# Kernel tuning notes

Measured on AMD Instinct MI355X. Metric: run time of the kernel, lower is better.

Reference implementation:

```python
import jax, jax.numpy as jnp
import numpy as np

TIME_LAG, PRE_LEN, STATIONS, SAMPLES = 12, 3, 40, 38
B, H, DM, DFF = 4, 8, 512, 2048
L = STATIONS * SAMPLES          # 1520 tokens fed to Informer
SAMPLE_K = 40                   # factor(5)*ceil(ln L); also n_top selected queries
N_ENC = 2


def sinusoid(length, d):
    pos = np.arange(length, dtype=np.float32)[:, None]
    i = np.arange(d)[None, :]
    ang = pos / np.power(10000.0, (2 * (i // 2)) / d)
    pe = np.where(i % 2 == 0, np.sin(ang), np.cos(ang)).astype(np.float32)
    return jnp.asarray(pe)


def layernorm(x, g, b, eps=1e-5):
    mu = x.mean(-1, keepdims=True)
    var = ((x - mu) ** 2).mean(-1, keepdims=True)
    return (x - mu) * jax.lax.rsqrt(var + eps) * g + b


def heads(x):
    b, l, d = x.shape
    return x.reshape(b, l, H, d // H).transpose(0, 2, 1, 3)


def unheads(x):
    b, h, l, dh = x.shape
    return x.transpose(0, 2, 1, 3).reshape(b, l, h * dh)


def prob_attention(Q, K, V, idx):
    # ProbSparse attention (Informer). Q,K,V: [B,H,L,Dh]; idx: [L, SAMPLE_K] sampled key ids.
    b, h, l, dh = Q.shape
    def col(ic):  # one sampled key per query; avoids [B,H,L,S,Dh] gather blowup
        return jnp.einsum('bhld,bhld->bhl', Q, K[:, :, ic, :])
    qk_s = jnp.moveaxis(jax.lax.map(col, idx.T), 0, -1)       # [B,H,L,SAMPLE_K]
    M = qk_s.max(-1) - qk_s.sum(-1) / l                        # sparsity measure
    _, top = jax.lax.top_k(M, SAMPLE_K)                        # [B,H,n_top]
    Qr = jnp.take_along_axis(Q, top[..., None], axis=2)        # [B,H,n_top,Dh]
    scores = jnp.einsum('bhud,bhkd->bhuk', Qr, K) / jnp.sqrt(jnp.float32(dh))
    ctx_top = jax.nn.softmax(scores, axis=-1) @ V              # [B,H,n_top,Dh]
    ctx = jnp.broadcast_to(V.mean(axis=2, keepdims=True), Q.shape)
    bi = jnp.arange(b)[:, None, None]
    hi = jnp.arange(h)[None, :, None]
    return ctx.at[bi, hi, top].set(ctx_top)


def full_attention(Q, K, V):
    scores = jnp.einsum('bhqd,bhkd->bhqk', Q, K) / jnp.sqrt(jnp.float32(Q.shape[-1]))
    return jax.nn.softmax(scores, axis=-1) @ V


def ffn(x, Wa, ba, Wb, bb):
    return jax.nn.gelu(x @ Wa + ba) @ Wb + bb


def _forward(inflow, P, samp_idx):
    x = inflow[:, 2:2 + TIME_LAG].reshape(B, -1, TIME_LAG)     # [B,L,T] (row-major, same as torch)
    pe = sinusoid(L, DM)
    enc = x @ P['W_emb_e'] + P['b_emb_e'] + pe
    for i in range(N_ENC):
        qkv = enc @ P['enc_Wqkv'][i] + P['enc_bqkv'][i]
        q, k, v = jnp.split(qkv, 3, axis=-1)
        ctx = unheads(prob_attention(heads(q), heads(k), heads(v), samp_idx[i]))
        enc = layernorm(enc + ctx @ P['enc_Wo'][i] + P['enc_bo'][i], P['enc_ln1_g'][i], P['enc_ln1_b'][i])
        y = ffn(enc, P['enc_Wf1'][i], P['enc_bf1'][i], P['enc_Wf2'][i], P['enc_bf2'][i])
        enc = layernorm(enc + y, P['enc_ln2_g'][i], P['enc_ln2_b'][i])
    enc = layernorm(enc, P['enc_norm_g'], P['enc_norm_b'])
    dec = x @ P['W_emb_d'] + P['b_emb_d'] + pe
    qkv = dec @ P['dec_Wqkv'] + P['dec_bqkv']
    q, k, v = jnp.split(qkv, 3, axis=-1)
    ctx = unheads(prob_attention(heads(q), heads(k), heads(v), samp_idx[2]))
    dec = layernorm(dec + ctx @ P['dec_Wo_s'] + P['dec_bo_s'], P['dec_ln1_g'], P['dec_ln1_b'])
    qc = dec @ P['dec_Wq_c'] + P['dec_bq_c']
    kc, vc = jnp.split(enc @ P['dec_Wkv_c'] + P['dec_bkv_c'], 2, axis=-1)
    ctx = unheads(full_attention(heads(qc), heads(kc), heads(vc)))
    dec = layernorm(dec + ctx @ P['dec_Wo_c'] + P['dec_bo_c'], P['dec_ln2_g'], P['dec_ln2_b'])
    y = ffn(dec, P['dec_Wf1'], P['dec_bf1'], P['dec_Wf2'], P['dec_bf2'])
    dec = layernorm(dec + y, P['dec_ln3_g'], P['dec_ln3_b'])
    out = dec @ P['W_proj'] + P['b_proj'] + x                  # Informer output + residual
    out = jax.nn.relu(out @ P['W1'] + P['b1']) @ P['W3'] + P['b3']
    return out.reshape(B, PRE_LEN, STATIONS, SAMPLES)


def setup_inputs():
    key = jax.random.key(0)
    keys = iter(jax.random.split(key, 80))
    def w(*shape):
        return jax.random.normal(next(keys), shape, jnp.float32) * 0.02
    def zeros(*shape):
        return jnp.zeros(shape, jnp.float32)
    def ones(*shape):
        return jnp.ones(shape, jnp.float32)
    inp = dict(
        flow=zeros(1), ODRate=zeros(1), adj=zeros(1), external=zeros(1),
        inflow=jax.random.normal(next(keys), (B, 2 + TIME_LAG, STATIONS, SAMPLES), jnp.float32),
        W_emb_e=w(TIME_LAG, DM), b_emb_e=zeros(DM),
        W_emb_d=w(TIME_LAG, DM), b_emb_d=zeros(DM),
        enc_Wqkv=w(N_ENC, DM, 3 * DM), enc_bqkv=zeros(N_ENC, 3 * DM),
        enc_Wo=w(N_ENC, DM, DM), enc_bo=zeros(N_ENC, DM),
        enc_ln1_g=ones(N_ENC, DM), enc_ln1_b=zeros(N_ENC, DM),
        enc_Wf1=w(N_ENC, DM, DFF), enc_bf1=zeros(N_ENC, DFF),
        enc_Wf2=w(N_ENC, DFF, DM), enc_bf2=zeros(N_ENC, DM),
        enc_ln2_g=ones(N_ENC, DM), enc_ln2_b=zeros(N_ENC, DM),
        enc_norm_g=ones(DM), enc_norm_b=zeros(DM),
        dec_Wqkv=w(DM, 3 * DM), dec_bqkv=zeros(3 * DM),
        dec_Wo_s=w(DM, DM), dec_bo_s=zeros(DM),
        dec_ln1_g=ones(DM), dec_ln1_b=zeros(DM),
        dec_Wq_c=w(DM, DM), dec_bq_c=zeros(DM),
        dec_Wkv_c=w(DM, 2 * DM), dec_bkv_c=zeros(2 * DM),
        dec_Wo_c=w(DM, DM), dec_bo_c=zeros(DM),
        dec_ln2_g=ones(DM), dec_ln2_b=zeros(DM),
        dec_Wf1=w(DM, DFF), dec_bf1=zeros(DFF),
        dec_Wf2=w(DFF, DM), dec_bf2=zeros(DM),
        dec_ln3_g=ones(DM), dec_ln3_b=zeros(DM),
        W_proj=w(DM, TIME_LAG), b_proj=zeros(TIME_LAG),
        W1=w(TIME_LAG, 128), b1=zeros(128),
        W3=w(128, PRE_LEN), b3=zeros(PRE_LEN),
        samp_idx=jax.random.randint(next(keys), (3, L, SAMPLE_K), 0, L, jnp.int32),
    )
    return inp


def reference(flow, inflow, ODRate, adj, external, W_emb_e, b_emb_e, W_emb_d, b_emb_d, enc_Wqkv, enc_bqkv, enc_Wo, enc_bo, enc_ln1_g, enc_ln1_b, enc_Wf1, enc_bf1, enc_Wf2, enc_bf2, enc_ln2_g, enc_ln2_b, enc_norm_g, enc_norm_b, dec_Wqkv, dec_bqkv, dec_Wo_s, dec_bo_s, dec_ln1_g, dec_ln1_b, dec_Wq_c, dec_bq_c, dec_Wkv_c, dec_bkv_c, dec_Wo_c, dec_bo_c, dec_ln2_g, dec_ln2_b, dec_Wf1, dec_bf1, dec_Wf2, dec_bf2, dec_ln3_g, dec_ln3_b, W_proj, b_proj, W1, b1, W3, b3, samp_idx):
    args = locals()
    skip = ('flow', 'inflow', 'ODRate', 'adj', 'external', 'samp_idx')
    P = {k: v for k, v in args.items() if k not in skip}
    return _forward(inflow, P, samp_idx)
```

## Files before the change

kernel.cpp:

```cpp
#include <hip/hip_runtime.h>
#include <math.h>

#define B_ 4
#define H_ 8
#define L_ 1520
#define DM_ 512
#define DFF_ 2048
#define SK_ 40
#define ML_ (B_*L_)
#define MP_ 6144
#define LP_ 1536

typedef unsigned short u16;
typedef short s8v __attribute__((ext_vector_type(8)));
typedef float f4 __attribute__((ext_vector_type(4)));

__device__ __forceinline__ u16 f2b(float x) {
  union { float f; unsigned u; } c; c.f = x;
  unsigned r = c.u + 0x7FFFu + ((c.u >> 16) & 1u);
  return (u16)(r >> 16);
}
__device__ __forceinline__ float b2f(u16 h) {
  union { unsigned u; float f; } c; c.u = ((unsigned)h) << 16;
  return c.f;
}
__device__ __forceinline__ unsigned cvt_pk(float a, float b) {
  unsigned r;
  asm volatile("v_cvt_pk_bf16_f32 %0, %1, %2" : "=v"(r) : "v"(a), "v"(b));
  return r;
}
__device__ __forceinline__ float gelu_tanh(float x) {
  float x3 = x * x * x;
  return 0.5f * x * (1.f + tanhf(0.79788456080286536f * (x + 0.044715f * x3)));
}
__device__ __forceinline__ int xswz(int bid, int cpx) {
  return (bid & 7) * cpx + (bid >> 3);
}

__global__ __launch_bounds__(256) void pe_kernel(float* __restrict__ pe) {
  int idx = blockIdx.x * 256 + threadIdx.x;
  if (idx >= L_ * DM_) return;
  int pos = idx / DM_, i = idx % DM_;
  double expo = (double)(2 * (i / 2)) / (double)DM_;
  double ang = (double)pos / pow(10000.0, expo);
  pe[idx] = (i & 1) ? (float)cos(ang) : (float)sin(ang);
}

__global__ __launch_bounds__(256) void extract_x(const float* __restrict__ inflow,
                                                 float* __restrict__ X) {
  int idx = blockIdx.x * 256 + threadIdx.x;
  if (idx >= ML_ * 12) return;
  int b = idx / (L_ * 12);
  int rem = idx - b * (L_ * 12);
  X[idx] = inflow[(size_t)b * 14 * L_ + 2 * L_ + rem];
}

struct CvtArgs {
  const float* src[15];
  unsigned cumt[16];
  unsigned lk[15];
};
__global__ __launch_bounds__(256) void cvt_all(CvtArgs a, u16* __restrict__ dst) {
  __shared__ float tl[32][33];
  int bt = blockIdx.x;
  int s = 0;
#pragma unroll
  for (int i = 1; i < 15; ++i) s += (bt >= (int)a.cumt[i]);
  int lt = bt - a.cumt[s];
  unsigned lk = a.lk[s];
  unsigned K = 1u << lk;
  unsigned N = ((a.cumt[s + 1] - a.cumt[s]) << 10) >> lk;
  unsigned tiles_n = N >> 5;
  unsigned k0 = (lt / tiles_n) * 32, n0 = (lt % tiles_n) * 32;
  const float* src = a.src[s];
  int r = threadIdx.x >> 5, c = threadIdx.x & 31;
#pragma unroll
  for (int i = 0; i < 4; ++i)
    tl[r + 8 * i][c] = src[(size_t)(k0 + r + 8 * i) * N + n0 + c];
  __syncthreads();
  u16* d = dst + ((size_t)a.cumt[s] << 10);
#pragma unroll
  for (int i = 0; i < 4; ++i)
    d[(size_t)(n0 + r + 8 * i) * K + k0 + c] = f2b(tl[c][r + 8 * i]);
}

__global__ __launch_bounds__(256) void embed_fused(
    const float* __restrict__ X, const float* __restrict__ W,
    const float* __restrict__ bias, const float* __restrict__ PE,
    float* __restrict__ ACT, u16* __restrict__ ACTb) {
  int row = blockIdx.x * 4 + (threadIdx.x >> 6);
  int lane = threadIdx.x & 63;
  int d0 = lane * 8;
  if (row >= ML_) {
    s8v z = {0, 0, 0, 0, 0, 0, 0, 0};
    *(s8v*)(ACTb + (size_t)row * DM_ + d0) = z;
    return;
  }
  int prow = row % L_;
  f4 a0 = *(const f4*)(bias + d0);
  f4 a1 = *(const f4*)(bias + d0 + 4);
  a0 += *(const f4*)(PE + (size_t)prow * DM_ + d0);
  a1 += *(const f4*)(PE + (size_t)prow * DM_ + d0 + 4);
  const float* xr = X + (size_t)row * 12;
#pragma unroll
  for (int t = 0; t < 12; ++t) {
    float xv = xr[t];
    a0 += xv * *(const f4*)(W + (size_t)t * DM_ + d0);
    a1 += xv * *(const f4*)(W + (size_t)t * DM_ + d0 + 4);
  }
  float* dst = ACT + (size_t)row * DM_ + d0;
  *(f4*)dst = a0;
  *(f4*)(dst + 4) = a1;
  unsigned ob[4];
  ob[0] = cvt_pk(a0[0], a0[1]); ob[1] = cvt_pk(a0[2], a0[3]);
  ob[2] = cvt_pk(a1[0], a1[1]); ob[3] = cvt_pk(a1[2], a1[3]);
  *(s8v*)(ACTb + (size_t)row * DM_ + d0) = *(s8v*)ob;
}

__global__ __launch_bounds__(256) void head_fused(
    const float* __restrict__ DEC, const float* __restrict__ X,
    const float* __restrict__ Wp, const float* __restrict__ bp,
    const float* __restrict__ W1, const float* __restrict__ b1,
    const float* __restrict__ W3, const float* __restrict__ b3,
    float* __restrict__ out) {
  int row = blockIdx.x * 4 + (threadIdx.x >> 6);
  int lane = threadIdx.x & 63;
  int d0 = lane * 8;
  const float* dec = DEC + (size_t)row * DM_ + d0;
  f4 v0 = *(const f4*)dec;
  f4 v1 = *(const f4*)(dec + 4);
  float pj[12];
#pragma unroll
  for (int j = 0; j < 12; ++j) pj[j] = 0.f;
#pragma unroll
  for (int i = 0; i < 8; ++i) {
    float dv = (i < 4) ? v0[i] : v1[i - 4];
    const float* wr = Wp + (size_t)(d0 + i) * 12;
#pragma unroll
    for (int j = 0; j < 12; ++j) pj[j] += dv * wr[j];
  }
  for (int off = 32; off; off >>= 1) {
#pragma unroll
    for (int j = 0; j < 12; ++j) pj[j] += __shfl_xor(pj[j], off);
  }
  float o12[12];
#pragma unroll
  for (int j = 0; j < 12; ++j) o12[j] = pj[j] + bp[j] + X[(size_t)row * 12 + j];
  int k0 = lane * 2;
  float h0 = b1[k0], h1 = b1[k0 + 1];
#pragma unroll
  for (int j = 0; j < 12; ++j) {
    h0 += o12[j] * W1[j * 128 + k0];
    h1 += o12[j] * W1[j * 128 + k0 + 1];
  }
  h0 = fmaxf(h0, 0.f);
  h1 = fmaxf(h1, 0.f);
  float op[3];
#pragma unroll
  for (int p = 0; p < 3; ++p)
    op[p] = h0 * W3[k0 * 3 + p] + h1 * W3[(k0 + 1) * 3 + p];
  for (int off = 32; off; off >>= 1) {
#pragma unroll
    for (int p = 0; p < 3; ++p) op[p] += __shfl_xor(op[p], off);
  }
  if (lane == 0) {
#pragma unroll
    for (int p = 0; p < 3; ++p) out[(size_t)row * 3 + p] = op[p] + b3[p];
  }
}

template<int BM>
__global__ __launch_bounds__(256) void gemm_bf16(
    const u16* __restrict__ A, const u16* __restrict__ Bt,
    const float* __restrict__ bias, const float* __restrict__ res,
    float* __restrict__ Cf, u16* __restrict__ Cb,
    int N, int K, int act) {
  __shared__ __align__(16) u16 As[BM * 32];
  __shared__ __align__(16) u16 Bs[128 * 32];
  constexpr int MI = BM / 32;
  const int nwg = gridDim.x * gridDim.y;
  const int lin = blockIdx.y * gridDim.x + blockIdx.x;
  const int o = xswz(lin, nwg >> 3);
  const int bxi = o % gridDim.x, byi = o / gridDim.x;
  const int t = threadIdx.x, w = t >> 6, lane = t & 63;
  const int lg = lane >> 4, li = lane & 15;
  const int bm = byi * BM, bn = bxi * 128;
  const int wr = (w >> 1) * (BM / 2), wc = (w & 1) * 64;
  f4 acc[MI][4];
#pragma unroll
  for (int i = 0; i < MI; ++i)
#pragma unroll
    for (int j = 0; j < 4; ++j) acc[i][j] = f4{0.f, 0.f, 0.f, 0.f};
  const int rB = w * 32 + (lane >> 2);
  const int rA = (BM == 128) ? rB : (w * 16 + (lane >> 2));
  const int ps = lane & 3;
  for (int k0 = 0; k0 < K; k0 += 32) {
    if (BM == 128) {
#pragma unroll
      for (int j = 0; j < 2; ++j) {
        int r = rA + j * 16;
        int ls = ps ^ ((r >> 1) & 3);
        __builtin_amdgcn_global_load_lds(
            (const __attribute__((address_space(1))) void*)(A + (size_t)(bm + r) * K + k0 + ls * 8),
            (__attribute__((address_space(3))) void*)(As + (w * 32 + j * 16) * 32),
            16, 0, 0);
      }
    } else {
      int ls = ps ^ ((rA >> 1) & 3);
      __builtin_amdgcn_global_load_lds(
          (const __attribute__((address_space(1))) void*)(A + (size_t)(bm + rA) * K + k0 + ls * 8),
          (__attribute__((address_space(3))) void*)(As + (w * 16) * 32),
          16, 0, 0);
    }
#pragma unroll
    for (int j = 0; j < 2; ++j) {
      int r = rB + j * 16;
      int ls = ps ^ ((r >> 1) & 3);
      __builtin_amdgcn_global_load_lds(
          (const __attribute__((address_space(1))) void*)(Bt + (size_t)(bn + r) * K + k0 + ls * 8),
          (__attribute__((address_space(3))) void*)(Bs + (w * 32 + j * 16) * 32),
          16, 0, 0);
    }
    __syncthreads();
    s8v af[MI], bf[4];
#pragma unroll
    for (int f = 0; f < MI; ++f) {
      int ra = wr + f * 16 + li;
      af[f] = *(const s8v*)(As + ra * 32 + ((lg ^ ((ra >> 1) & 3)) * 8));
    }
#pragma unroll
    for (int f = 0; f < 4; ++f) {
      int rb = wc + f * 16 + li;
      bf[f] = *(const s8v*)(Bs + rb * 32 + ((lg ^ ((rb >> 1) & 3)) * 8));
    }
#pragma unroll
    for (int fi = 0; fi < MI; ++fi)
#pragma unroll
      for (int fj = 0; fj < 4; ++fj)
        acc[fi][fj] = __builtin_amdgcn_mfma_f32_16x16x32_bf16(af[fi], bf[fj], acc[fi][fj], 0, 0, 0);
    __syncthreads();
  }
#pragma unroll
  for (int fi = 0; fi < MI; ++fi)
#pragma unroll
    for (int fj = 0; fj < 4; ++fj)
#pragma unroll
      for (int r = 0; r < 4; ++r) {
        int row = bm + wr + fi * 16 + lg * 4 + r;
        int col = bn + wc + fj * 16 + li;
        float v = acc[fi][fj][r] + bias[col];
        if (res && row < ML_) v += res[(size_t)row * N + col];
        if (act == 1) v = gelu_tanh(v);
        if (Cf && row < ML_) Cf[(size_t)row * N + col] = v;
        if (Cb) Cb[(size_t)row * N + col] = f2b(v);
      }
}

__global__ __launch_bounds__(256) void layernorm_ip(float* __restrict__ Xb,
                                                    const float* __restrict__ g,
                                                    const float* __restrict__ bta,
                                                    u16* __restrict__ outb) {
  int row = blockIdx.x * 4 + (threadIdx.x >> 6);
  int lane = threadIdx.x & 63;
  float* x = Xb + (size_t)row * DM_;
  f4 a = *(f4*)(x + lane * 8);
  f4 b = *(f4*)(x + lane * 8 + 4);
  float s = a[0] + a[1] + a[2] + a[3] + b[0] + b[1] + b[2] + b[3];
  for (int off = 32; off; off >>= 1) s += __shfl_xor(s, off);
  float mu = s * (1.f / 512.f);
  float vs = 0.f;
#pragma unroll
  for (int i = 0; i < 4; ++i) { a[i] -= mu; b[i] -= mu; vs += a[i] * a[i] + b[i] * b[i]; }
  for (int off = 32; off; off >>= 1) vs += __shfl_xor(vs, off);
  float rs = rsqrtf(vs * (1.f / 512.f) + 1e-5f);
  f4 g0 = *(const f4*)(g + lane * 8), g1 = *(const f4*)(g + lane * 8 + 4);
  f4 c0 = *(const f4*)(bta + lane * 8), c1 = *(const f4*)(bta + lane * 8 + 4);
  float r0 = a[0] * rs * g0[0] + c0[0];
  float r1 = a[1] * rs * g0[1] + c0[1];
  float r2 = a[2] * rs * g0[2] + c0[2];
  float r3 = a[3] * rs * g0[3] + c0[3];
  float r4 = b[0] * rs * g1[0] + c1[0];
  float r5 = b[1] * rs * g1[1] + c1[1];
  float r6 = b[2] * rs * g1[2] + c1[2];
  float r7 = b[3] * rs * g1[3] + c1[3];
  x[lane * 8 + 0] = r0; x[lane * 8 + 1] = r1; x[lane * 8 + 2] = r2; x[lane * 8 + 3] = r3;
  x[lane * 8 + 4] = r4; x[lane * 8 + 5] = r5; x[lane * 8 + 6] = r6; x[lane * 8 + 7] = r7;
  unsigned ob[4];
  ob[0] = cvt_pk(r0, r1); ob[1] = cvt_pk(r2, r3);
  ob[2] = cvt_pk(r4, r5); ob[3] = cvt_pk(r6, r7);
  *(s8v*)(outb + (size_t)row * DM_ + lane * 8) = *(s8v*)ob;
}

__global__ __launch_bounds__(256) void probM(const u16* __restrict__ qkv,
                                             const int* __restrict__ sidx,
                                             float* __restrict__ Mout) {
  int wid = threadIdx.x / 64, lane = threadIdx.x % 64;
  int o = xswz(blockIdx.x, (B_ * H_ * L_ / 4) >> 3);
  int g = o * 4 + wid;
  int l = g % L_;
  int bh = g / L_;
  int h = bh % H_, b = bh / H_;
  __shared__ float qs[4][64];
  qs[wid][lane] = b2f(qkv[((size_t)b * L_ + l) * 1536 + h * 64 + lane]);
  __syncthreads();
  float dot = 0.f;
  if (lane < SK_) {
    int ks = sidx[l * SK_ + lane];
    const u16* kr = qkv + ((size_t)b * L_ + ks) * 1536 + 512 + h * 64;
#pragma unroll
    for (int j = 0; j < 8; ++j) {
      s8v v = *(const s8v*)(kr + j * 8);
#pragma unroll
      for (int i = 0; i < 8; ++i) dot += qs[wid][j * 8 + i] * b2f((u16)v[i]);
    }
  }
  float vmax = (lane < SK_) ? dot : -INFINITY;
  float vsum = (lane < SK_) ? dot : 0.f;
  for (int off = 32; off; off >>= 1) {
    vmax = fmaxf(vmax, __shfl_xor(vmax, off));
    vsum += __shfl_xor(vsum, off);
  }
  if (lane == 0) Mout[g] = vmax - vsum / (float)L_;
}

__global__ __launch_bounds__(256) void radix_topk(const float* __restrict__ Mv,
                                                  int* __restrict__ top) {
  const int bh = blockIdx.x;
  const int t = threadIdx.x;
  const int base = t * 6;
  unsigned key[6];
#pragma unroll
  for (int i = 0; i < 6; ++i) {
    int ix = base + i;
    unsigned k = 0u;
    if (ix < L_) {
      union { float f; unsigned u; } c; c.f = Mv[(size_t)bh * L_ + ix];
      k = c.u ^ ((c.u & 0x80000000u) ? 0xFFFFFFFFu : 0x80000000u);
    }
    key[i] = k;
  }
  __shared__ int wred[4];
  __shared__ int s_a[256], s_b[256];
  unsigned prefix = 0u;
  for (int b = 31; b >= 0; --b) {
    unsigned cand = prefix | (1u << b);
    int c = 0;
#pragma unroll
    for (int i = 0; i < 6; ++i) c += (key[i] >= cand);
    for (int off = 32; off; off >>= 1) c += __shfl_xor(c, off);
    if ((t & 63) == 0) wred[t >> 6] = c;
    __syncthreads();
    int tot = wred[0] + wred[1] + wred[2] + wred[3];
    if (tot >= SK_) prefix = cand;
    __syncthreads();
  }
  const unsigned T = prefix;
  int gt = 0, tie = 0;
#pragma unroll
  for (int i = 0; i < 6; ++i) { gt += (key[i] > T); tie += (key[i] == T); }
  s_a[t] = gt; s_b[t] = tie;
  __syncthreads();
  for (int off = 1; off < 256; off <<= 1) {
    int va = (t >= off) ? s_a[t - off] : 0;
    int vb = (t >= off) ? s_b[t - off] : 0;
    __syncthreads();
    s_a[t] += va; s_b[t] += vb;
    __syncthreads();
  }
  const int n_strict = s_a[255];
  const int gt_base = s_a[t] - gt;
  const int tie_base = s_b[t] - tie;
  const int need = SK_ - n_strict;
  int lgt = 0, ltie = 0;
#pragma unroll
  for (int i = 0; i < 6; ++i) {
    int ix = base + i;
    if (key[i] > T) {
      top[bh * SK_ + gt_base + lgt] = ix; ++lgt;
    } else if (key[i] == T) {
      int r = tie_base + ltie; ++ltie;
      if (r < need) top[bh * SK_ + n_strict + r] = ix;
    }
  }
}

__global__ __launch_bounds__(256) void transpose_v(const u16* __restrict__ src,
                                                   int stride, int voff0,
                                                   u16* __restrict__ VT) {
  int o = xswz(blockIdx.x, (B_ * H_ * 24) >> 3);
  int kt = o % 24, bh = o / 24;
  int h = bh & 7, b = bh >> 3;
  int kb = kt * 64;
  __shared__ u16 tile[64][72];
  int t = threadIdx.x;
#pragma unroll
  for (int rr = 0; rr < 2; ++rr) {
    int slot = rr * 256 + t;
    int key = slot >> 3, d = (slot & 7) * 8;
    int gk = kb + key; if (gk >= L_) gk = L_ - 1;
    s8v v = *(const s8v*)(src + (size_t)(b * L_ + gk) * stride + voff0 + h * 64 + d);
    *(s8v*)(&tile[key][d]) = v;
  }
  __syncthreads();
  int dim = t >> 2, k0 = (t & 3) * 16;
  u16 buf[16];
#pragma unroll
  for (int i = 0; i < 16; ++i) {
    int key = k0 + i;
    buf[i] = (kb + key < L_) ? tile[key][dim] : (u16)0;
  }
  *(s8v*)(VT + ((size_t)bh * 64 + dim) * LP_ + kb + k0) = *(s8v*)buf;
  *(s8v*)(VT + ((size_t)bh * 64 + dim) * LP_ + kb + k0 + 8) = *(s8v*)(buf + 8);
}

template<int MODE>
__global__ __launch_bounds__(256) void flash_attn(
    const u16* __restrict__ Qm, const u16* __restrict__ Kg,
    const u16* __restrict__ VT, const int* __restrict__ top,
    float* __restrict__ POf, u16* POa, u16* POb,
    float* __restrict__ PM, float* __restrict__ PL) {
  constexpr int QSTR = (MODE == 0) ? 512 : 1536;
  constexpr int KSTR = (MODE == 0) ? 512 : 1536;
  constexpr int TILES = (MODE == 0) ? 12 : 3;
  constexpr int NB = (MODE == 0) ? 48 : 8;
  __shared__ __align__(16) u16 Kt[64 * 64];
  __shared__ __align__(16) u16 Vt[64 * 64];
  __shared__ __align__(16) unsigned Xch[4][576];
  const int o = xswz(blockIdx.x, (B_ * H_ * NB) >> 3);
  int bh, sp, qb;
  if (MODE == 0) {
    bh = o / 48; int rem = o % 48; qb = rem >> 1; sp = rem & 1;
  } else {
    bh = o / 8; sp = o % 8; qb = 0;
  }
  const int h = bh & 7, b = bh >> 3;
  const int qoff = h * 64;
  const int koff = ((MODE == 0) ? 0 : 512) + h * 64;
  const int t = threadIdx.x, w = t >> 6, lane = t & 63;
  const int lg = lane >> 4, li = lane & 15;
  const u16* vtg = VT + (size_t)bh * 64 * LP_;
  unsigned* xw = Xch[w];
  u16* xw16 = (u16*)xw;

  int qrow;
  if (MODE == 0) {
    int q = qb * 64 + w * 16 + li;
    qrow = b * L_ + ((q < L_) ? q : (L_ - 1));
  } else {
    int u = w * 16 + li; if (u >= SK_) u = SK_ - 1;
    qrow = b * L_ + top[bh * SK_ + u];
  }
  s8v qf0 = *(const s8v*)(Qm + (size_t)qrow * QSTR + qoff + lg * 8);
  s8v qf1 = *(const s8v*)(Qm + (size_t)qrow * QSTR + qoff + 32 + lg * 8);

  f4 o4[4];
#pragma unroll
  for (int n = 0; n < 4; ++n) o4[n] = f4{0.f, 0.f, 0.f, 0.f};
  float m_run = -INFINITY, l_run = 0.f;
  const int kt0 = sp * TILES;
  const int skey = lane >> 3;
  const int sslot = lane & 7;

#pragma unroll 1
  for (int ki = 0; ki < TILES; ++ki) {
    const int kb = (kt0 + ki) * 64;
#pragma unroll
    for (int j = 0; j < 2; ++j) {
      int row = w * 16 + j * 8 + skey;
      int gk = kb + row; if (gk >= L_) gk = L_ - 1;
      int ck = sslot ^ (row & 7);
      __builtin_amdgcn_global_load_lds(
          (const __attribute__((address_space(1))) void*)(Kg + (size_t)(b * L_ + gk) * KSTR + koff + ck * 8),
          (__attribute__((address_space(3))) void*)(Kt + (w * 16 + j * 8) * 64),
          16, 0, 0);
      int cv = sslot ^ (row & 7);
      __builtin_amdgcn_global_load_lds(
          (const __attribute__((address_space(1))) void*)(vtg + (size_t)row * LP_ + kb + cv * 8),
          (__attribute__((address_space(3))) void*)(Vt + (w * 16 + j * 8) * 64),
          16, 0, 0);
    }
    __syncthreads();
    f4 s[4];
#pragma unroll
    for (int c = 0; c < 4; ++c) {
      int key = c * 16 + li;
      s8v kf = *(const s8v*)(Kt + key * 64 + ((lg ^ (key & 7)) * 8));
      s8v kg2 = *(const s8v*)(Kt + key * 64 + (((lg + 4) ^ (key & 7)) * 8));
      f4 z = f4{0.f, 0.f, 0.f, 0.f};
      z = __builtin_amdgcn_mfma_f32_16x16x32_bf16(kf, qf0, z, 0, 0, 0);
      z = __builtin_amdgcn_mfma_f32_16x16x32_bf16(kg2, qf1, z, 0, 0, 0);
      s[c] = z * 0.125f;
    }
    if (kb + 64 > L_) {
#pragma unroll
      for (int c = 0; c < 4; ++c)
#pragma unroll
        for (int r = 0; r < 4; ++r)
          if (kb + c * 16 + lg * 4 + r >= L_) s[c][r] = -INFINITY;
    }
    float tm = -INFINITY;
#pragma unroll
    for (int c = 0; c < 4; ++c)
      tm = fmaxf(tm, fmaxf(fmaxf(s[c][0], s[c][1]), fmaxf(s[c][2], s[c][3])));
    tm = fmaxf(tm, __shfl_xor(tm, 16));
    tm = fmaxf(tm, __shfl_xor(tm, 32));
    float mn = fmaxf(m_run, tm);
    float sc = __expf(m_run - mn);
    float p[4][4];
    float rs = 0.f;
#pragma unroll
    for (int c = 0; c < 4; ++c)
#pragma unroll
      for (int r = 0; r < 4; ++r) { p[c][r] = __expf(s[c][r] - mn); rs += p[c][r]; }
    rs += __shfl_xor(rs, 16);
    rs += __shfl_xor(rs, 32);
    l_run = l_run * sc + rs;
    m_run = mn;
#pragma unroll
    for (int n = 0; n < 4; ++n) o4[n] *= sc;
#pragma unroll
    for (int c = 0; c < 4; ++c)
#pragma unroll
      for (int rp = 0; rp < 2; ++rp)
        xw[li * 36 + c * 8 + lg * 2 + rp] = cvt_pk(p[c][2 * rp], p[c][2 * rp + 1]);
    s8v pb0 = *(const s8v*)(xw + li * 36 + lg * 4);
    s8v pb1 = *(const s8v*)(xw + li * 36 + 16 + lg * 4);
#pragma unroll
    for (int n = 0; n < 4; ++n) {
      int dim = n * 16 + li;
      s8v vb0 = *(const s8v*)(Vt + dim * 64 + ((lg ^ (dim & 7)) * 8));
      o4[n] = __builtin_amdgcn_mfma_f32_16x16x32_bf16(vb0, pb0, o4[n], 0, 0, 0);
    }
#pragma unroll
    for (int n = 0; n < 4; ++n) {
      int dim = n * 16 + li;
      s8v vb1 = *(const s8v*)(Vt + dim * 64 + (((lg + 4) ^ (dim & 7)) * 8));
      o4[n] = __builtin_amdgcn_mfma_f32_16x16x32_bf16(vb1, pb1, o4[n], 0, 0, 0);
    }
    __syncthreads();
  }

  if (MODE == 0) {
#pragma unroll
    for (int n = 0; n < 4; ++n)
#pragma unroll
      for (int rp = 0; rp < 2; ++rp)
        xw[li * 36 + n * 8 + lg * 2 + rp] = cvt_pk(o4[n][2 * rp], o4[n][2 * rp + 1]);
    u16* PO = sp ? POb : POa;
    const int pid = (bh * 24 + qb) * 2 + sp;
    int q_local = lane >> 2, d0 = (lane & 3) * 16;
    int q = qb * 64 + w * 16 + q_local;
    s8v v0 = *(const s8v*)(xw16 + q_local * 72 + d0);
    s8v v1 = *(const s8v*)(xw16 + q_local * 72 + d0 + 8);
    if (q < L_) {
      u16* dst = PO + ((size_t)(b * L_ + q)) * DM_ + qoff + d0;
      *(s8v*)dst = v0;
      *(s8v*)(dst + 8) = v1;
    }
    if (lg == 0) {
      PM[pid * 64 + w * 16 + li] = m_run;
      PL[pid * 64 + w * 16 + li] = l_run;
    }
  } else {
    int base = (bh * 8 + sp) * 64 + w * 16 + li;
#pragma unroll
    for (int n = 0; n < 4; ++n)
#pragma unroll
      for (int r = 0; r < 4; ++r)
        POf[(size_t)base * 64 + n * 16 + lg * 4 + r] = o4[n][r];
    if (lg == 0) {
      PM[base] = m_run;
      PL[base] = l_run;
    }
  }
}

__global__ __launch_bounds__(256) void combine_cross(const u16* __restrict__ PO0,
                                                     const float* __restrict__ PM,
                                                     const float* __restrict__ PL,
                                                     u16* ctxb) {
  int idx = blockIdx.x * 256 + threadIdx.x;
  int row = idx >> 9, col = idx & 511;
  int b = row / L_, q = row - b * L_;
  int h = col >> 6;
  int bh = b * 8 + h, qbk = q >> 6, qi = q & 63;
  int p0 = ((bh * 24 + qbk) * 2) * 64 + qi;
  float m0 = PM[p0], m1 = PM[p0 + 64];
  float l0 = PL[p0], l1 = PL[p0 + 64];
  float M = fmaxf(m0, m1);
  float w0 = __expf(m0 - M), w1 = __expf(m1 - M);
  float inv = 1.f / (w0 * l0 + w1 * l1);
  float o0 = b2f(PO0[idx]);
  float o1 = b2f(ctxb[idx]);
  ctxb[idx] = f2b((w0 * o0 + w1 * o1) * inv);
}

__global__ __launch_bounds__(256) void combine_prob_scatter(
    const float* __restrict__ PO, const float* __restrict__ PM,
    const float* __restrict__ PL, const int* __restrict__ top,
    u16* __restrict__ ctxb) {
  int bh = blockIdx.x;
  int t = threadIdx.x;
  int u = t >> 2, dg = (t & 3) * 16;
  if (u >= SK_) return;
  float M = -INFINITY;
  for (int s = 0; s < 8; ++s) M = fmaxf(M, PM[(bh * 8 + s) * 64 + u]);
  float wgt[8];
  float den = 0.f;
  for (int s = 0; s < 8; ++s) {
    wgt[s] = __expf(PM[(bh * 8 + s) * 64 + u] - M);
    den += wgt[s] * PL[(bh * 8 + s) * 64 + u];
  }
  float inv = 1.f / den;
  int h = bh & 7, b = bh >> 3;
  int l = top[bh * SK_ + u];
  u16* dst = ctxb + ((size_t)(b * L_ + l)) * DM_ + h * 64;
  for (int d = dg; d < dg + 16; ++d) {
    float acc = 0.f;
    for (int s = 0; s < 8; ++s) acc += wgt[s] * PO[(((size_t)bh * 8 + s) * 64 + u) * 64 + d];
    dst[d] = f2b(acc * inv);
  }
}

__global__ __launch_bounds__(256) void vmean_part(const u16* __restrict__ qkv,
                                                  float* __restrict__ part) {
  int g = xswz(blockIdx.x, (B_ * H_ * 8) >> 3);
  int bh = g >> 3, seg = g & 7;
  int h = bh & 7, b = bh >> 3;
  int lane = threadIdx.x & 63, grp = threadIdx.x >> 6;
  int k0 = seg * 190, k1 = k0 + 190;
  float acc = 0.f;
  for (int k = k0 + grp; k < k1; k += 4)
    acc += b2f(qkv[((size_t)b * L_ + k) * 1536 + 1024 + h * 64 + lane]);
  __shared__ float pv[4][64];
  pv[grp][lane] = acc;
  __syncthreads();
  if (threadIdx.x < 64)
    part[g * 64 + threadIdx.x] =
        pv[0][threadIdx.x] + pv[1][threadIdx.x] + pv[2][threadIdx.x] + pv[3][threadIdx.x];
}

__global__ __launch_bounds__(256) void fill_ctx(const float* __restrict__ part,
                                                u16* __restrict__ ctxb) {
  int idx = blockIdx.x * 256 + threadIdx.x;
  int d = idx % 64;
  int h = (idx / 64) % H_;
  int b = idx / (L_ * DM_);
  int bh = b * 8 + h;
  float s = 0.f;
#pragma unroll
  for (int seg = 0; seg < 8; ++seg) s += part[(bh * 8 + seg) * 64 + d];
  ctxb[idx] = f2b(s * (1.f / (float)L_));
}

extern "C" void kernel_launch(void* const* d_in, const int* in_sizes, int n_in,
                              void* d_out, int out_size, void* d_ws, size_t ws_size,
                              hipStream_t stream) {
  const float* inflow   = (const float*)d_in[4];
  const float* W_emb_e  = (const float*)d_in[5];
  const float* b_emb_e  = (const float*)d_in[6];
  const float* W_emb_d  = (const float*)d_in[7];
  const float* b_emb_d  = (const float*)d_in[8];
  const float* enc_Wqkv = (const float*)d_in[9];
  const float* enc_bqkv = (const float*)d_in[10];
  const float* enc_Wo   = (const float*)d_in[11];
  const float* enc_bo   = (const float*)d_in[12];
  const float* enc_ln1g = (const float*)d_in[13];
  const float* enc_ln1b = (const float*)d_in[14];
  const float* enc_Wf1  = (const float*)d_in[15];
  const float* enc_bf1  = (const float*)d_in[16];
  const float* enc_Wf2  = (const float*)d_in[17];
  const float* enc_bf2  = (const float*)d_in[18];
  const float* enc_ln2g = (const float*)d_in[19];
  const float* enc_ln2b = (const float*)d_in[20];
  const float* enc_ng   = (const float*)d_in[21];
  const float* enc_nb   = (const float*)d_in[22];
  const float* dec_Wqkv = (const float*)d_in[23];
  const float* dec_bqkv = (const float*)d_in[24];
  const float* dec_Wo_s = (const float*)d_in[25];
  const float* dec_bo_s = (const float*)d_in[26];
  const float* dec_ln1g = (const float*)d_in[27];
  const float* dec_ln1b = (const float*)d_in[28];
  const float* dec_Wq_c = (const float*)d_in[29];
  const float* dec_bq_c = (const float*)d_in[30];
  const float* dec_Wkv  = (const float*)d_in[31];
  const float* dec_bkv  = (const float*)d_in[32];
  const float* dec_Wo_c = (const float*)d_in[33];
  const float* dec_bo_c = (const float*)d_in[34];
  const float* dec_ln2g = (const float*)d_in[35];
  const float* dec_ln2b = (const float*)d_in[36];
  const float* dec_Wf1  = (const float*)d_in[37];
  const float* dec_bf1  = (const float*)d_in[38];
  const float* dec_Wf2  = (const float*)d_in[39];
  const float* dec_bf2  = (const float*)d_in[40];
  const float* dec_ln3g = (const float*)d_in[41];
  const float* dec_ln3b = (const float*)d_in[42];
  const float* W_proj   = (const float*)d_in[43];
  const float* b_proj   = (const float*)d_in[44];
  const float* W1       = (const float*)d_in[45];
  const float* b1       = (const float*)d_in[46];
  const float* W3       = (const float*)d_in[47];
  const float* b3       = (const float*)d_in[48];
  const int*   samp     = (const int*)d_in[49];
  float* out = (float*)d_out;

  float* ws  = (float*)d_ws;
  float* PE  = ws;
  float* X   = PE + 778240;
  float* ACT = X + 72960;
  float* REG = ACT + 3112960;
  float* MME = REG + 6291456;
  float* CTT = MME + 48640;
  float* VME = CTT + 81920;
  int*   TOP = (int*)(VME + 2048);
  float* TAIL = VME + 2048 + 1280;
  u16* ENCb = (u16*)TAIL;
  u16* DECb = (u16*)(TAIL + 1572864);
  u16* CTXb = (u16*)(TAIL + 2 * 1572864);
  u16* WBF  = (u16*)(TAIL + 3 * 1572864);
  float* POp = (float*)(WBF + 10485760);
  float* PMp = POp + 1048576;
  float* PLp = PMp + 16384;

  u16* QKVb = (u16*)REG;
  u16* FFb  = (u16*)REG;
  u16* VT   = (u16*)REG + 9437184;
  u16* QCb  = (u16*)REG;
  u16* Kc   = (u16*)REG + 3145728;
  u16* Vc   = (u16*)REG + 6291456;
  float* PMc = PE;
  float* PLc = PE + 98304;
  float* VME8 = MME;

  auto GB = [&](const u16* A, const u16* Bt, const float* bias, const float* res,
                float* Cf, u16* Cb, int N, int K, int act) {
    if (N <= 512) {
      dim3 g(N / 128, MP_ / 64);
      gemm_bf16<64><<<g, 256, 0, stream>>>(A, Bt, bias, res, Cf, Cb, N, K, act);
    } else {
      dim3 g(N / 128, MP_ / 128);
      gemm_bf16<128><<<g, 256, 0, stream>>>(A, Bt, bias, res, Cf, Cb, N, K, act);
    }
  };
  auto PROB = [&](const int* sidx) {
    probM<<<B_ * H_ * L_ / 4, 256, 0, stream>>>(QKVb, sidx, MME);
    radix_topk<<<B_ * H_, 256, 0, stream>>>(MME, TOP);
    transpose_v<<<B_ * H_ * 24, 256, 0, stream>>>(QKVb, 1536, 1024, VT);
    flash_attn<1><<<B_ * H_ * 8, 256, 0, stream>>>(QKVb, QKVb, VT, TOP, POp,
                                                   nullptr, nullptr, PMp, PLp);
    vmean_part<<<B_ * H_ * 8, 256, 0, stream>>>(QKVb, VME8);
    fill_ctx<<<ML_ * DM_ / 256, 256, 0, stream>>>(VME8, CTXb);
    combine_prob_scatter<<<B_ * H_, 256, 0, stream>>>(POp, PMp, PLp, TOP, CTXb);
  };

  pe_kernel<<<(L_ * DM_ + 255) / 256, 256, 0, stream>>>(PE);
  extract_x<<<(ML_ * 12 + 255) / 256, 256, 0, stream>>>(inflow, X);

  {
    CvtArgs a;
    const float* s[15] = {
      enc_Wqkv, enc_Wqkv + 512 * 1536, enc_Wo, enc_Wo + 512 * 512,
      enc_Wf1, enc_Wf1 + 512 * 2048, enc_Wf2, enc_Wf2 + 2048 * 512,
      dec_Wqkv, dec_Wo_s, dec_Wq_c, dec_Wkv, dec_Wo_c, dec_Wf1, dec_Wf2 };
    unsigned cumt[16] = { 0u, 768u, 1536u, 1792u, 2048u, 3072u,
                          4096u, 5120u, 6144u, 6912u, 7168u,
                          7424u, 7936u, 8192u, 9216u, 10240u };
    unsigned lk[15] = { 9, 9, 9, 9, 9, 9, 11, 11, 9, 9, 9, 9, 9, 9, 11 };
    for (int i = 0; i < 15; ++i) { a.src[i] = s[i]; a.lk[i] = lk[i]; }
    for (int i = 0; i < 16; ++i) a.cumt[i] = cumt[i];
    cvt_all<<<10240, 256, 0, stream>>>(a, WBF);
  }
  u16* Wt_qkv_e0 = WBF + 0;
  u16* Wt_qkv_e1 = WBF + 786432;
  u16* Wt_o_e0   = WBF + 1572864;
  u16* Wt_o_e1   = WBF + 1835008;
  u16* Wt_f1_e0  = WBF + 2097152;
  u16* Wt_f1_e1  = WBF + 3145728;
  u16* Wt_f2_e0  = WBF + 4194304;
  u16* Wt_f2_e1  = WBF + 5242880;
  u16* Wt_qkv_d  = WBF + 6291456;
  u16* Wt_o_s    = WBF + 7077888;
  u16* Wt_q_c    = WBF + 7340032;
  u16* Wt_kv_c   = WBF + 7602176;
  u16* Wt_o_c    = WBF + 8126464;
  u16* Wt_f1_d   = WBF + 8388608;
  u16* Wt_f2_d   = WBF + 9437184;

  embed_fused<<<MP_ / 4, 256, 0, stream>>>(X, W_emb_e, b_emb_e, PE, ACT, ENCb);

  const u16* Wqkv_e[2] = {Wt_qkv_e0, Wt_qkv_e1};
  const u16* Wo_e[2]   = {Wt_o_e0, Wt_o_e1};
  const u16* Wf1_e[2]  = {Wt_f1_e0, Wt_f1_e1};
  const u16* Wf2_e[2]  = {Wt_f2_e0, Wt_f2_e1};
  for (int i = 0; i < 2; ++i) {
    GB(ENCb, Wqkv_e[i], enc_bqkv + i * 1536, nullptr, nullptr, QKVb, 1536, 512, 0);
    PROB(samp + (size_t)i * L_ * SK_);
    GB(CTXb, Wo_e[i], enc_bo + i * 512, ACT, ACT, nullptr, 512, 512, 0);
    layernorm_ip<<<ML_ / 4, 256, 0, stream>>>(ACT, enc_ln1g + i * 512, enc_ln1b + i * 512, ENCb);
    GB(ENCb, Wf1_e[i], enc_bf1 + i * 2048, nullptr, nullptr, FFb, 2048, 512, 1);
    GB(FFb, Wf2_e[i], enc_bf2 + i * 512, ACT, ACT, nullptr, 512, 2048, 0);
    layernorm_ip<<<ML_ / 4, 256, 0, stream>>>(ACT, enc_ln2g + i * 512, enc_ln2b + i * 512, ENCb);
  }
  layernorm_ip<<<ML_ / 4, 256, 0, stream>>>(ACT, enc_ng, enc_nb, ENCb);

  embed_fused<<<MP_ / 4, 256, 0, stream>>>(X, W_emb_d, b_emb_d, PE, ACT, DECb);
  GB(DECb, Wt_qkv_d, dec_bqkv, nullptr, nullptr, QKVb, 1536, 512, 0);
  PROB(samp + (size_t)2 * L_ * SK_);
  GB(CTXb, Wt_o_s, dec_bo_s, ACT, ACT, nullptr, 512, 512, 0);
  layernorm_ip<<<ML_ / 4, 256, 0, stream>>>(ACT, dec_ln1g, dec_ln1b, DECb);

  GB(DECb, Wt_q_c, dec_bq_c, nullptr, nullptr, QCb, 512, 512, 0);
  GB(ENCb, Wt_kv_c, dec_bkv, nullptr, nullptr, Kc, 512, 512, 0);
  GB(ENCb, Wt_kv_c + 512 * 512, dec_bkv + 512, nullptr, nullptr, Vc, 512, 512, 0);
  transpose_v<<<B_ * H_ * 24, 256, 0, stream>>>(Vc, 512, 0, VT);
  flash_attn<0><<<B_ * H_ * 48, 256, 0, stream>>>(QCb, Kc, VT, nullptr, nullptr,
                                                  Vc, CTXb, PMc, PLc);
  combine_cross<<<ML_ * DM_ / 256, 256, 0, stream>>>(Vc, PMc, PLc, CTXb);
  GB(CTXb, Wt_o_c, dec_bo_c, ACT, ACT, nullptr, 512, 512, 0);
  layernorm_ip<<<ML_ / 4, 256, 0, stream>>>(ACT, dec_ln2g, dec_ln2b, DECb);

  GB(DECb, Wt_f1_d, dec_bf1, nullptr, nullptr, FFb, 2048, 512, 1);
  GB(FFb, Wt_f2_d, dec_bf2, ACT, ACT, nullptr, 512, 2048, 0);
  layernorm_ip<<<ML_ / 4, 256, 0, stream>>>(ACT, dec_ln3g, dec_ln3b, DECb);

  head_fused<<<ML_ / 4, 256, 0, stream>>>(ACT, X, W_proj, b_proj, W1, b1, W3, b3, out);
}
```

Measured before the change: 869.4 us.

## Fuse V-mean into transpose, merge cross K/V GEMM, add lazy softmax rescale

The V column sums are now computed inside the transpose_v kernel as per-tile partials, which removes the separate vmean_part pass over V. The two cross-attention K and V projection GEMMs become one N=1024 GEMM writing an interleaved KV buffer, and the flash kernel's K stride is updated to match. The online softmax now skips the rescale of the running max and accumulators unless some lane's tile max exceeds the running max by more than 8, which saves exp and multiply work per tile. The cost is fill_ctx summing 24 partials instead of 8, a separate partial-output buffer for cross attention, and a looser bound on exp values under the lazy rescale.

```diff
diff --git a/kernel.cpp b/kernel.cpp
--- a/kernel.cpp
+++ b/kernel.cpp
@@ -386,7 +386,8 @@
 
 __global__ __launch_bounds__(256) void transpose_v(const u16* __restrict__ src,
                                                    int stride, int voff0,
-                                                   u16* __restrict__ VT) {
+                                                   u16* __restrict__ VT,
+                                                   float* __restrict__ vpart) {
   int o = xswz(blockIdx.x, (B_ * H_ * 24) >> 3);
   int kt = o % 24, bh = o / 24;
   int h = bh & 7, b = bh >> 3;
@@ -404,13 +405,20 @@
   __syncthreads();
   int dim = t >> 2, k0 = (t & 3) * 16;
   u16 buf[16];
+  float psum = 0.f;
 #pragma unroll
   for (int i = 0; i < 16; ++i) {
     int key = k0 + i;
     buf[i] = (kb + key < L_) ? tile[key][dim] : (u16)0;
+    psum += b2f(buf[i]);
   }
   *(s8v*)(VT + ((size_t)bh * 64 + dim) * LP_ + kb + k0) = *(s8v*)buf;
   *(s8v*)(VT + ((size_t)bh * 64 + dim) * LP_ + kb + k0 + 8) = *(s8v*)(buf + 8);
+  if (vpart) {
+    psum += __shfl_xor(psum, 1);
+    psum += __shfl_xor(psum, 2);
+    if ((t & 3) == 0) vpart[((size_t)bh * 24 + kt) * 64 + dim] = psum;
+  }
 }
 
 template<int MODE>
@@ -420,7 +428,7 @@
     float* __restrict__ POf, u16* POa, u16* POb,
     float* __restrict__ PM, float* __restrict__ PL) {
   constexpr int QSTR = (MODE == 0) ? 512 : 1536;
-  constexpr int KSTR = (MODE == 0) ? 512 : 1536;
+  constexpr int KSTR = (MODE == 0) ? 1024 : 1536;
   constexpr int TILES = (MODE == 0) ? 12 : 3;
   constexpr int NB = (MODE == 0) ? 48 : 8;
   __shared__ __align__(16) u16 Kt[64 * 64];
@@ -504,20 +512,23 @@
       tm = fmaxf(tm, fmaxf(fmaxf(s[c][0], s[c][1]), fmaxf(s[c][2], s[c][3])));
     tm = fmaxf(tm, __shfl_xor(tm, 16));
     tm = fmaxf(tm, __shfl_xor(tm, 32));
-    float mn = fmaxf(m_run, tm);
-    float sc = __expf(m_run - mn);
+    if (!__all(tm <= m_run + 8.f)) {
+      float mn = fmaxf(m_run, tm);
+      float sc = __expf(m_run - mn);
+      l_run *= sc;
+      m_run = mn;
+#pragma unroll
+      for (int n = 0; n < 4; ++n) o4[n] *= sc;
+    }
     float p[4][4];
     float rs = 0.f;
 #pragma unroll
     for (int c = 0; c < 4; ++c)
 #pragma unroll
-      for (int r = 0; r < 4; ++r) { p[c][r] = __expf(s[c][r] - mn); rs += p[c][r]; }
+      for (int r = 0; r < 4; ++r) { p[c][r] = __expf(s[c][r] - m_run); rs += p[c][r]; }
     rs += __shfl_xor(rs, 16);
     rs += __shfl_xor(rs, 32);
-    l_run = l_run * sc + rs;
-    m_run = mn;
-#pragma unroll
-    for (int n = 0; n < 4; ++n) o4[n] *= sc;
+    l_run += rs;
 #pragma unroll
     for (int c = 0; c < 4; ++c)
 #pragma unroll
@@ -622,24 +633,6 @@
   }
 }
 
-__global__ __launch_bounds__(256) void vmean_part(const u16* __restrict__ qkv,
-                                                  float* __restrict__ part) {
-  int g = xswz(blockIdx.x, (B_ * H_ * 8) >> 3);
-  int bh = g >> 3, seg = g & 7;
-  int h = bh & 7, b = bh >> 3;
-  int lane = threadIdx.x & 63, grp = threadIdx.x >> 6;
-  int k0 = seg * 190, k1 = k0 + 190;
-  float acc = 0.f;
-  for (int k = k0 + grp; k < k1; k += 4)
-    acc += b2f(qkv[((size_t)b * L_ + k) * 1536 + 1024 + h * 64 + lane]);
-  __shared__ float pv[4][64];
-  pv[grp][lane] = acc;
-  __syncthreads();
-  if (threadIdx.x < 64)
-    part[g * 64 + threadIdx.x] =
-        pv[0][threadIdx.x] + pv[1][threadIdx.x] + pv[2][threadIdx.x] + pv[3][threadIdx.x];
-}
-
 __global__ __launch_bounds__(256) void fill_ctx(const float* __restrict__ part,
                                                 u16* __restrict__ ctxb) {
   int idx = blockIdx.x * 256 + threadIdx.x;
@@ -649,7 +642,7 @@
   int bh = b * 8 + h;
   float s = 0.f;
 #pragma unroll
-  for (int seg = 0; seg < 8; ++seg) s += part[(bh * 8 + seg) * 64 + d];
+  for (int seg = 0; seg < 24; ++seg) s += part[((size_t)bh * 24 + seg) * 64 + d];
   ctxb[idx] = f2b(s * (1.f / (float)L_));
 }
 
@@ -721,16 +714,16 @@
   float* POp = (float*)(WBF + 10485760);
   float* PMp = POp + 1048576;
   float* PLp = PMp + 16384;
+  u16*   PO0 = (u16*)(PLp + 16384);
 
   u16* QKVb = (u16*)REG;
   u16* FFb  = (u16*)REG;
   u16* VT   = (u16*)REG + 9437184;
   u16* QCb  = (u16*)REG;
-  u16* Kc   = (u16*)REG + 3145728;
-  u16* Vc   = (u16*)REG + 6291456;
+  u16* KVCb = (u16*)REG + 3145728;
   float* PMc = PE;
   float* PLc = PE + 98304;
-  float* VME8 = MME;
+  float* VME24 = CTT;
 
   auto GB = [&](const u16* A, const u16* Bt, const float* bias, const float* res,
                 float* Cf, u16* Cb, int N, int K, int act) {
@@ -745,11 +738,10 @@
   auto PROB = [&](const int* sidx) {
     probM<<<B_ * H_ * L_ / 4, 256, 0, stream>>>(QKVb, sidx, MME);
     radix_topk<<<B_ * H_, 256, 0, stream>>>(MME, TOP);
-    transpose_v<<<B_ * H_ * 24, 256, 0, stream>>>(QKVb, 1536, 1024, VT);
+    transpose_v<<<B_ * H_ * 24, 256, 0, stream>>>(QKVb, 1536, 1024, VT, VME24);
     flash_attn<1><<<B_ * H_ * 8, 256, 0, stream>>>(QKVb, QKVb, VT, TOP, POp,
                                                    nullptr, nullptr, PMp, PLp);
-    vmean_part<<<B_ * H_ * 8, 256, 0, stream>>>(QKVb, VME8);
-    fill_ctx<<<ML_ * DM_ / 256, 256, 0, stream>>>(VME8, CTXb);
+    fill_ctx<<<ML_ * DM_ / 256, 256, 0, stream>>>(VME24, CTXb);
     combine_prob_scatter<<<B_ * H_, 256, 0, stream>>>(POp, PMp, PLp, TOP, CTXb);
   };
 
@@ -810,12 +802,11 @@
   layernorm_ip<<<ML_ / 4, 256, 0, stream>>>(ACT, dec_ln1g, dec_ln1b, DECb);
 
   GB(DECb, Wt_q_c, dec_bq_c, nullptr, nullptr, QCb, 512, 512, 0);
-  GB(ENCb, Wt_kv_c, dec_bkv, nullptr, nullptr, Kc, 512, 512, 0);
-  GB(ENCb, Wt_kv_c + 512 * 512, dec_bkv + 512, nullptr, nullptr, Vc, 512, 512, 0);
-  transpose_v<<<B_ * H_ * 24, 256, 0, stream>>>(Vc, 512, 0, VT);
-  flash_attn<0><<<B_ * H_ * 48, 256, 0, stream>>>(QCb, Kc, VT, nullptr, nullptr,
-                                                  Vc, CTXb, PMc, PLc);
-  combine_cross<<<ML_ * DM_ / 256, 256, 0, stream>>>(Vc, PMc, PLc, CTXb);
+  GB(ENCb, Wt_kv_c, dec_bkv, nullptr, nullptr, KVCb, 1024, 512, 0);
+  transpose_v<<<B_ * H_ * 24, 256, 0, stream>>>(KVCb, 1024, 512, VT, nullptr);
+  flash_attn<0><<<B_ * H_ * 48, 256, 0, stream>>>(QCb, KVCb, VT, nullptr, nullptr,
+                                                  PO0, CTXb, PMc, PLc);
+  combine_cross<<<ML_ * DM_ / 256, 256, 0, stream>>>(PO0, PMc, PLc, CTXb);
   GB(CTXb, Wt_o_c, dec_bo_c, ACT, ACT, nullptr, 512, 512, 0);
   layernorm_ip<<<ML_ / 4, 256, 0, stream>>>(ACT, dec_ln2g, dec_ln2b, DECb);
 
```

Result: no change. 859.8 us (-1.1%).
